# Performance work log

Hardware: AMD Instinct MI355X
Metric: run time of the kernel (lower is better)

Reference implementation:

```python
import jax, jax.numpy as jnp
import numpy as np

H = 3  # hidden size (matches nn.LSTM(3, 3, ...))


def _lstm_dir(x, Wih, Whh, bih, bhh, reverse):
    """One direction of one LSTM layer. x: [B,T,D]; PyTorch gate order i,f,g,o."""
    B = x.shape[0]
    xT = jnp.swapaxes(x, 0, 1)  # [T,B,D]
    # Precompute input projection for all timesteps (memory-bound GEMM once).
    x_proj = jnp.einsum('tbd,gd->tbg', xT, Wih) + (bih + bhh)  # [T,B,4H]

    def step(carry, xp):
        h, c = carry
        gates = xp + h @ Whh.T  # [B,4H]
        i = jax.nn.sigmoid(gates[:, :H])
        f = jax.nn.sigmoid(gates[:, H:2 * H])
        g = jnp.tanh(gates[:, 2 * H:3 * H])
        o = jax.nn.sigmoid(gates[:, 3 * H:])
        c = f * c + i * g
        h = o * jnp.tanh(c)
        return (h, c), h

    init = (jnp.zeros((B, H), x.dtype), jnp.zeros((B, H), x.dtype))
    _, hs = jax.lax.scan(step, init, x_proj, reverse=reverse)
    return jnp.swapaxes(hs, 0, 1)  # [B,T,H], time-aligned with input


def setup_inputs() -> dict:
    key = jax.random.key(0)
    ks = jax.random.split(key, 20)
    B, T = 8192, 512
    k = 1.0 / np.sqrt(H)

    def u(kk, shape):
        return jax.random.uniform(kk, shape, jnp.float32, -k, k)

    inp = {"x": jax.random.normal(ks[0], (B, T, 3), jnp.float32)}
    # layer 0: input dim 3; layer 1: input dim 2*H = 6
    inp.update({
        "W_ih_l0": u(ks[1], (4 * H, 3)),  "W_hh_l0": u(ks[2], (4 * H, H)),
        "b_ih_l0": u(ks[3], (4 * H,)),    "b_hh_l0": u(ks[4], (4 * H,)),
        "W_ih_l0r": u(ks[5], (4 * H, 3)), "W_hh_l0r": u(ks[6], (4 * H, H)),
        "b_ih_l0r": u(ks[7], (4 * H,)),   "b_hh_l0r": u(ks[8], (4 * H,)),
        "W_ih_l1": u(ks[9], (4 * H, 2 * H)),  "W_hh_l1": u(ks[10], (4 * H, H)),
        "b_ih_l1": u(ks[11], (4 * H,)),       "b_hh_l1": u(ks[12], (4 * H,)),
        "W_ih_l1r": u(ks[13], (4 * H, 2 * H)),"W_hh_l1r": u(ks[14], (4 * H, H)),
        "b_ih_l1r": u(ks[15], (4 * H,)),      "b_hh_l1r": u(ks[16], (4 * H,)),
        "W_lin": u(ks[17], (1, 2 * H)),       "b_lin": u(ks[18], (1,)),
    })
    return inp


def reference(x, W_ih_l0, W_hh_l0, b_ih_l0, b_hh_l0,
              W_ih_l0r, W_hh_l0r, b_ih_l0r, b_hh_l0r,
              W_ih_l1, W_hh_l1, b_ih_l1, b_hh_l1,
              W_ih_l1r, W_hh_l1r, b_ih_l1r, b_hh_l1r,
              W_lin, b_lin):
    # layer 0 (bidirectional)
    y0 = jnp.concatenate([
        _lstm_dir(x, W_ih_l0, W_hh_l0, b_ih_l0, b_hh_l0, False),
        _lstm_dir(x, W_ih_l0r, W_hh_l0r, b_ih_l0r, b_hh_l0r, True),
    ], axis=-1)  # [B,T,6]
    # layer 1 (bidirectional)
    y1 = jnp.concatenate([
        _lstm_dir(y0, W_ih_l1, W_hh_l1, b_ih_l1, b_hh_l1, False),
        _lstm_dir(y0, W_ih_l1r, W_hh_l1r, b_ih_l1r, b_hh_l1r, True),
    ], axis=-1)  # [B,T,6]
    last = y1[:, -1, :]  # [B,6]  (output sequence at final timestep)
    out = last @ W_lin.T + b_lin  # [B,1]
    return jax.nn.sigmoid(out.reshape(-1))  # [B]
```

## Files before the change

### kernel.cpp

```cpp
#include <hip/hip_runtime.h>


#define B_ 8192
#define T_ 512
#define LOG2E 1.4426950408889634f

typedef float v2f __attribute__((ext_vector_type(2)));

__device__ __forceinline__ float rcp_(float x)  { return __builtin_amdgcn_rcpf(x); }
__device__ __forceinline__ float exp2_(float x) { return __builtin_amdgcn_exp2f(x); }
__device__ __forceinline__ float sigm_(float x) {
  return rcp_(1.0f + exp2_(-LOG2E * x));
}
__device__ __forceinline__ float tanh_(float x) {
  return 1.0f - 2.0f * rcp_(1.0f + exp2_(2.0f * LOG2E * x));
}
__device__ __forceinline__ float act_(float p) { return rcp_(1.f + exp2_(p)); }

__device__ __forceinline__ v2f sp(float s) { return (v2f){s, s}; }
__device__ __forceinline__ v2f pkfma(v2f a, float b, v2f c) {
  return __builtin_elementwise_fma(a, sp(b), c);
}

#define PIN2(v) do {                                                      \
    double _d = __builtin_bit_cast(double, v);                            \
    asm volatile("" : "+v"(_d));                                          \
    v = __builtin_bit_cast(v2f, _d); } while (0)

template <int CTRL>
__device__ __forceinline__ float dppf(float v) {
  int s = __float_as_int(v);
  return __int_as_float(__builtin_amdgcn_update_dpp(s, s, CTRL, 0xF, 0xF, false));
}
#define QP0 dppf<0x00>
#define QP1 dppf<0x55>
#define QP2 dppf<0xAA>
#define SHL4 0x104
#define SHR4 0x114

template <bool DIRB>
__device__ __forceinline__ void l0_dir(
    const float* __restrict__ x,
    const float* __restrict__ Wi, const float* __restrict__ Wh,
    const float* __restrict__ bi, const float* __restrict__ bh,
    float* __restrict__ yout, int b, int lane)
{
  bool qgo = (lane & 4) != 0;
  int j = lane & 3; int jj = (j < 3) ? j : 0;
  const int ra = (qgo ? 6 : 0) + jj, rb = ra + 3;
  const float kx = qgo ? (-2.f * LOG2E) : (-LOG2E);
  const float ky = -LOG2E;
  const float avx = qgo ? 2.f : 1.f;
  const float dvx = qgo ? -1.f : 0.f;

  v2f w0 = {Wi[ra*3+0]*kx, Wi[rb*3+0]*ky},
      w1 = {Wi[ra*3+1]*kx, Wi[rb*3+1]*ky},
      w2 = {Wi[ra*3+2]*kx, Wi[rb*3+2]*ky};
  v2f u0 = {Wh[ra*3+0]*kx, Wh[rb*3+0]*ky},
      u1 = {Wh[ra*3+1]*kx, Wh[rb*3+1]*ky},
      u2 = {Wh[ra*3+2]*kx, Wh[rb*3+2]*ky};
  v2f b2 = {(bi[ra]+bh[ra])*kx, (bi[rb]+bh[rb])*ky};

  float h = 0.f, c = 0.f, ha0 = 0.f, ha1 = 0.f, ha2 = 0.f;
  float hs0, hs1, hs2, hs3, hs4, hs5, hs6, hs7;

  const float4* xq = (const float4*)(x + (size_t)b * (T_ * 3));
  float* ywb = yout + (size_t)b * (T_ * 3) + jj * 8;

  float4 p0, p1, p2, p3, p4, p5, q0, q1, q2, q3, q4, q5;

#define LD1(blk, R0, R1, R2, R3, R4, R5) do {                             \
    const float4* _p = xq + (blk) * 6;                                    \
    R0 = _p[0]; R1 = _p[1]; R2 = _p[2];                                   \
    R3 = _p[3]; R4 = _p[4]; R5 = _p[5];                                   \
    __builtin_amdgcn_sched_barrier(0); } while (0)

#define STEP1(x0, x1, x2, HOUT) do {                                      \
    v2f pv = pkfma(w0, (x0), b2); pv = pkfma(w1, (x1), pv);               \
    pv = pkfma(w2, (x2), pv);                                             \
    v2f uv = u0 * sp(ha0); uv = pkfma(u1, ha1, uv);                       \
    uv = pkfma(u2, ha2, uv);                                              \
    pv = pv + uv;                                                         \
    float r0v = act_(pv.x);                                               \
    float ayv = act_(pv.y);                         \
    float axv = __builtin_fmaf(avx, r0v, dvx);  \
    float slx = dppf<SHL4>(axv), sly = dppf<SHL4>(ayv);                   \
    float srx = dppf<SHR4>(axv), sry = dppf<SHR4>(ayv);                   \
    float pig = axv * (qgo ? srx : slx);           \
    float gf  = qgo ? sry : ayv;                                          \
    float gO  = qgo ? ayv : sly;                                          \
    c = __builtin_fmaf(gf, c, pig);                                       \
    float th = __builtin_fmaf(                                            \
        2.f, rcp_(1.f + exp2_(-2.f * LOG2E * c)), -1.f);                  \
    h = gO * th;                                                          \
    ha0 = QP0(h); ha1 = QP1(h); ha2 = QP2(h);                             \
    HOUT = h; } while (0)

#define S0(R0,R1,R2,R3,R4,R5) STEP1(R0.x, R0.y, R0.z, hs0)
#define S1(R0,R1,R2,R3,R4,R5) STEP1(R0.w, R1.x, R1.y, hs1)
#define S2(R0,R1,R2,R3,R4,R5) STEP1(R1.z, R1.w, R2.x, hs2)
#define S3(R0,R1,R2,R3,R4,R5) STEP1(R2.y, R2.z, R2.w, hs3)
#define S4(R0,R1,R2,R3,R4,R5) STEP1(R3.x, R3.y, R3.z, hs4)
#define S5(R0,R1,R2,R3,R4,R5) STEP1(R3.w, R4.x, R4.y, hs5)
#define S6(R0,R1,R2,R3,R4,R5) STEP1(R4.z, R4.w, R5.x, hs6)
#define S7(R0,R1,R2,R3,R4,R5) STEP1(R5.y, R5.z, R5.w, hs7)

#define PROC1(R0,R1,R2,R3,R4,R5) do {                                     \
    if (DIRB) {                                                           \
      S7(R0,R1,R2,R3,R4,R5); S6(R0,R1,R2,R3,R4,R5);                       \
      S5(R0,R1,R2,R3,R4,R5); S4(R0,R1,R2,R3,R4,R5);                       \
      S3(R0,R1,R2,R3,R4,R5); S2(R0,R1,R2,R3,R4,R5);                       \
      S1(R0,R1,R2,R3,R4,R5); S0(R0,R1,R2,R3,R4,R5);                       \
    } else {                                                              \
      S0(R0,R1,R2,R3,R4,R5); S1(R0,R1,R2,R3,R4,R5);                       \
      S2(R0,R1,R2,R3,R4,R5); S3(R0,R1,R2,R3,R4,R5);                       \
      S4(R0,R1,R2,R3,R4,R5); S5(R0,R1,R2,R3,R4,R5);                       \
      S6(R0,R1,R2,R3,R4,R5); S7(R0,R1,R2,R3,R4,R5);                       \
    } } while (0)

#define FLUSH1(blk) do {                                                  \
    if (lane < 3) {                                                       \
      float4* _o = (float4*)(ywb + (blk) * 24);                           \
      _o[0] = make_float4(hs0, hs1, hs2, hs3);                            \
      _o[1] = make_float4(hs4, hs5, hs6, hs7);                            \
    } } while (0)

#define BLK(k) (DIRB ? (63 - (k)) : (k))

  LD1(BLK(0), p0, p1, p2, p3, p4, p5);
  LD1(BLK(1), q0, q1, q2, q3, q4, q5);
  for (int k = 0; k < 64; k += 2) {
    PROC1(p0, p1, p2, p3, p4, p5);
    FLUSH1(BLK(k));
    if (k + 2 < 64) LD1(BLK(k + 2), p0, p1, p2, p3, p4, p5);
    PROC1(q0, q1, q2, q3, q4, q5);
    FLUSH1(BLK(k + 1));
    if (k + 3 < 64) LD1(BLK(k + 3), q0, q1, q2, q3, q4, q5);
  }
#undef LD1
#undef STEP1
#undef S0
#undef S1
#undef S2
#undef S3
#undef S4
#undef S5
#undef S6
#undef S7
#undef PROC1
#undef FLUSH1
#undef BLK
}

__global__ __launch_bounds__(256, 2) void lstm_l0_pair(
    const float* __restrict__ x,
    const float* __restrict__ Wf_ih, const float* __restrict__ Wf_hh,
    const float* __restrict__ bf_ih, const float* __restrict__ bf_hh,
    const float* __restrict__ Wr_ih, const float* __restrict__ Wr_hh,
    const float* __restrict__ br_ih, const float* __restrict__ br_hh,
    float* __restrict__ y0f, float* __restrict__ y0b)
{
  int gid = blockIdx.x * 256 + threadIdx.x;
  const int nfwd = B_ * 8;
  if (gid < nfwd) {
    l0_dir<false>(x, Wf_ih, Wf_hh, bf_ih, bf_hh, y0f, gid >> 3, gid & 7);
  } else {
    int g2 = gid - nfwd;
    l0_dir<true>(x, Wr_ih, Wr_hh, br_ih, br_hh, y0b, g2 >> 3, g2 & 7);
  }
}

#define CELL_TAIL(HOUT)                                                   \
    float r0v = act_(pv.x);                                               \
    float ayv = act_(pv.y);                                               \
    float axv = __builtin_fmaf(avx, r0v, dvx);                            \
    float slx = dppf<SHL4>(axv), sly = dppf<SHL4>(ayv);                   \
    float srx = dppf<SHR4>(axv), sry = dppf<SHR4>(ayv);                   \
    float pig = axv * (qgo ? srx : slx);                                  \
    float gf  = qgo ? sry : ayv;                                          \
    float gO  = qgo ? ayv : sly;                                          \
    c = __builtin_fmaf(gf, c, pig);                                       \
    float th = __builtin_fmaf(                                            \
        2.f, rcp_(1.f + exp2_(-2.f * LOG2E * c)), -1.f);                  \
    h = gO * th;                                                          \
    ha0 = QP0(h); ha1 = QP1(h); ha2 = QP2(h);                             \
    HOUT = h;

__global__ __launch_bounds__(256) void lstm_l1_fwd(
    const float* __restrict__ Wih1, const float* __restrict__ Whh1,
    const float* __restrict__ bih1, const float* __restrict__ bhh1,
    const float* __restrict__ Wih1r,
    const float* __restrict__ bih1r, const float* __restrict__ bhh1r,
    const float* __restrict__ Wlin, const float* __restrict__ blin,
    const float* __restrict__ y0f, const float* __restrict__ y0b,
    float* __restrict__ out)
{
  int tid  = blockIdx.x * 256 + threadIdx.x;
  int b    = tid >> 3;
  int lane = tid & 7;
  bool qgo = (lane & 4) != 0;
  int j = lane & 3; int jj = (j < 3) ? j : 0;
  const int ra = (qgo ? 6 : 0) + jj, rb = ra + 3;
  const float kx = qgo ? (-2.f * LOG2E) : (-LOG2E);
  const float ky = -LOG2E;
  const float avx = qgo ? 2.f : 1.f;
  const float dvx = qgo ? -1.f : 0.f;

  v2f w0 = {Wih1[ra*6+0]*kx, Wih1[rb*6+0]*ky},
      w1 = {Wih1[ra*6+1]*kx, Wih1[rb*6+1]*ky},
      w2 = {Wih1[ra*6+2]*kx, Wih1[rb*6+2]*ky},
      w3 = {Wih1[ra*6+3]*kx, Wih1[rb*6+3]*ky},
      w4 = {Wih1[ra*6+4]*kx, Wih1[rb*6+4]*ky},
      w5 = {Wih1[ra*6+5]*kx, Wih1[rb*6+5]*ky};
  v2f u0 = {Whh1[ra*3+0]*kx, Whh1[rb*3+0]*ky},
      u1 = {Whh1[ra*3+1]*kx, Whh1[rb*3+1]*ky},
      u2 = {Whh1[ra*3+2]*kx, Whh1[rb*3+2]*ky};
  v2f b2 = {(bih1[ra]+bhh1[ra])*kx, (bih1[rb]+bhh1[rb])*ky};
  PIN2(w0); PIN2(w1); PIN2(w2); PIN2(w3); PIN2(w4); PIN2(w5);
  PIN2(u0); PIN2(u1); PIN2(u2); PIN2(b2);

  const float4* yfq = (const float4*)(y0f + (size_t)b * (T_ * 3));
  const float4* ybq = (const float4*)(y0b + (size_t)b * (T_ * 3));

  const float* ufp = y0f + (size_t)b * (T_ * 3) + 63 * 24 + 7;
  const float* ubp = y0b + (size_t)b * (T_ * 3) + 63 * 24 + 7;

  float h = 0.f, c = 0.f, ha0 = 0.f, ha1 = 0.f, ha2 = 0.f;
  float hs0, hs1, hs2, hs3, hs4, hs5, hs6, hs7;
  float4 pf0, pf1, pf2, pf3, pf4, pf5, pb0, pb1, pb2, pb3, pb4, pb5;
  float4 qf0, qf1, qf2, qf3, qf4, qf5, qb0, qb1, qb2, qb3, qb4, qb5;

#define LDB(blk, F0,F1,F2,F3,F4,F5, G0,G1,G2,G3,G4,G5) do {               \
    const float4* _f = yfq + (blk) * 6;                                   \
    const float4* _g = ybq + (blk) * 6;                                   \
    F0 = _f[0]; F1 = _f[1]; F2 = _f[2];                                   \
    F3 = _f[3]; F4 = _f[4]; F5 = _f[5];                                   \
    G0 = _g[0]; G1 = _g[1]; G2 = _g[2];                                   \
    G3 = _g[3]; G4 = _g[4]; G5 = _g[5];                                   \
    __builtin_amdgcn_sched_barrier(0); } while (0)

#define STEPB(f0, f1, f2, g0, g1, g2, HOUT) do {                          \
    v2f pv = pkfma(w0, (f0), b2); pv = pkfma(w1, (f1), pv);               \
    pv = pkfma(w2, (f2), pv);                                             \
    v2f nv = w3 * sp(g0); nv = pkfma(w4, (g1), nv);                       \
    nv = pkfma(w5, (g2), nv);                                             \
    v2f uv = u0 * sp(ha0); uv = pkfma(u1, ha1, uv);                       \
    uv = pkfma(u2, ha2, uv);                                              \
    pv = (pv + nv) + uv;                                                  \
    CELL_TAIL(HOUT) } while (0)

#define PROCB(F0,F1,F2,F3,F4,F5, G0,G1,G2,G3,G4,G5) do {                  \
    STEPB(F0.x, F2.x, F4.x,  G0.x, G2.x, G4.x, hs0);                      \
    STEPB(F0.y, F2.y, F4.y,  G0.y, G2.y, G4.y, hs1);                      \
    STEPB(F0.z, F2.z, F4.z,  G0.z, G2.z, G4.z, hs2);                      \
    STEPB(F0.w, F2.w, F4.w,  G0.w, G2.w, G4.w, hs3);                      \
    STEPB(F1.x, F3.x, F5.x,  G1.x, G3.x, G5.x, hs4);                      \
    STEPB(F1.y, F3.y, F5.y,  G1.y, G3.y, G5.y, hs5);                      \
    STEPB(F1.z, F3.z, F5.z,  G1.z, G3.z, G5.z, hs6);                      \
    STEPB(F1.w, F3.w, F5.w,  G1.w, G3.w, G5.w, hs7); } while (0)

  LDB(0, pf0,pf1,pf2,pf3,pf4,pf5, pb0,pb1,pb2,pb3,pb4,pb5);
  LDB(1, qf0,qf1,qf2,qf3,qf4,qf5, qb0,qb1,qb2,qb3,qb4,qb5);
  for (int it = 0; it < 32; ++it) {
    PROCB(pf0,pf1,pf2,pf3,pf4,pf5, pb0,pb1,pb2,pb3,pb4,pb5);
    if (it < 31) LDB(2*it+2, pf0,pf1,pf2,pf3,pf4,pf5, pb0,pb1,pb2,pb3,pb4,pb5);
    PROCB(qf0,qf1,qf2,qf3,qf4,qf5, qb0,qb1,qb2,qb3,qb4,qb5);
    if (it < 31) LDB(2*it+3, qf0,qf1,qf2,qf3,qf4,qf5, qb0,qb1,qb2,qb3,qb4,qb5);
  }
  (void)hs0; (void)hs1; (void)hs2; (void)hs3;
  (void)hs4; (void)hs5; (void)hs6; (void)hs7;

  float uf0 = ufp[0], uf1 = ufp[8], uf2 = ufp[16];
  float ub0 = ubp[0], ub1 = ubp[8], ub2 = ubp[16];

  float h1b;
  {
    v2f r0 = {Wih1r[ra*6+0]*kx, Wih1r[rb*6+0]*ky},
        r1 = {Wih1r[ra*6+1]*kx, Wih1r[rb*6+1]*ky},
        r2 = {Wih1r[ra*6+2]*kx, Wih1r[rb*6+2]*ky},
        r3 = {Wih1r[ra*6+3]*kx, Wih1r[rb*6+3]*ky},
        r4 = {Wih1r[ra*6+4]*kx, Wih1r[rb*6+4]*ky},
        r5 = {Wih1r[ra*6+5]*kx, Wih1r[rb*6+5]*ky};
    v2f br = {(bih1r[ra]+bhh1r[ra])*kx, (bih1r[rb]+bhh1r[rb])*ky};
    v2f qv = pkfma(r0, uf0, br); qv = pkfma(r1, uf1, qv);
    qv = pkfma(r2, uf2, qv);     qv = pkfma(r3, ub0, qv);
    qv = pkfma(r4, ub1, qv);     qv = pkfma(r5, ub2, qv);
    float r0v = act_(qv.x);
    float ayv = act_(qv.y);
    float axv = __builtin_fmaf(avx, r0v, dvx);
    float slx = dppf<SHL4>(axv), sly = dppf<SHL4>(ayv);
    float srx = dppf<SHR4>(axv);
    float gi = qgo ? srx : axv;
    float gG = qgo ? axv : slx;
    float gO = qgo ? ayv : sly;
    float cb = gi * gG;
    h1b = gO * tanh_(cb);
  }

  float part = 0.f;
  if (!qgo && j < 3) part = __builtin_fmaf(Wlin[j], h, Wlin[3 + j] * h1b);
  part += __shfl_xor(part, 1, 8);
  part += __shfl_xor(part, 2, 8);
  part += __shfl_xor(part, 4, 8);
  if (lane == 0) out[b] = sigm_(part + blin[0]);
#undef LDB
#undef STEPB
#undef PROCB
}

extern "C" void kernel_launch(void* const* d_in, const int* in_sizes, int n_in,
                              void* d_out, int out_size, void* d_ws, size_t ws_size,
                              hipStream_t stream) {
  const float* x        = (const float*)d_in[0];
  const float* W_ih_l0  = (const float*)d_in[1];
  const float* W_hh_l0  = (const float*)d_in[2];
  const float* b_ih_l0  = (const float*)d_in[3];
  const float* b_hh_l0  = (const float*)d_in[4];
  const float* W_ih_l0r = (const float*)d_in[5];
  const float* W_hh_l0r = (const float*)d_in[6];
  const float* b_ih_l0r = (const float*)d_in[7];
  const float* b_hh_l0r = (const float*)d_in[8];
  const float* W_ih_l1  = (const float*)d_in[9];
  const float* W_hh_l1  = (const float*)d_in[10];
  const float* b_ih_l1  = (const float*)d_in[11];
  const float* b_hh_l1  = (const float*)d_in[12];
  const float* W_ih_l1r = (const float*)d_in[13];
  const float* b_ih_l1r = (const float*)d_in[15];
  const float* b_hh_l1r = (const float*)d_in[16];
  const float* W_lin    = (const float*)d_in[17];
  const float* b_lin    = (const float*)d_in[18];

  float* y0f = (float*)d_ws;
  float* y0b = (float*)d_ws + (size_t)B_ * T_ * 3;
  float* out = (float*)d_out;

  lstm_l0_pair<<<(B_ * 8 * 2) / 256, 256, 0, stream>>>(
      x, W_ih_l0, W_hh_l0, b_ih_l0, b_hh_l0,
      W_ih_l0r, W_hh_l0r, b_ih_l0r, b_hh_l0r, y0f, y0b);

  lstm_l1_fwd<<<(B_ * 8) / 256, 256, 0, stream>>>(
      W_ih_l1, W_hh_l1, b_ih_l1, b_hh_l1,
      W_ih_l1r, b_ih_l1r, b_hh_l1r,
      W_lin, b_lin, y0f, y0b, out);
}
```

Before: 166.9 us.

## Distribute per-block inputs across 8 lanes and broadcast via ds_swizzle

Before, every lane of an 8-lane sequence group loaded the full 24-float block of inputs with float4 loads, which is redundant traffic and register pressure. Now each lane loads only its slice (3 floats per timestep in layer 0, one strided element per feature in layer 1), and each timestep's values are broadcast within the group using ds_swizzle. Layer-0 weights are also pinned in registers. This cuts global/L1 load volume and VGPR use, but adds swizzle latency (LDS-path crossbar ops) into the serial recurrence chain.

```diff
diff --git a/kernel.cpp b/kernel.cpp
--- a/kernel.cpp
+++ b/kernel.cpp
@@ -37,6 +37,12 @@
 #define QP2 dppf<0xAA>
 #define SHL4 0x104
 #define SHR4 0x114
+
+template <int S>
+__device__ __forceinline__ float swz8(float v) {
+  return __int_as_float(__builtin_amdgcn_ds_swizzle(
+      __float_as_int(v), (S << 5) | 0x18));
+}
 
 template <bool DIRB>
 __device__ __forceinline__ void l0_dir(
@@ -47,6 +53,7 @@
 {
   bool qgo = (lane & 4) != 0;
   int j = lane & 3; int jj = (j < 3) ? j : 0;
+  int sl = lane & 7;
   const int ra = (qgo ? 6 : 0) + jj, rb = ra + 3;
   const float kx = qgo ? (-2.f * LOG2E) : (-LOG2E);
   const float ky = -LOG2E;
@@ -60,19 +67,19 @@
       u1 = {Wh[ra*3+1]*kx, Wh[rb*3+1]*ky},
       u2 = {Wh[ra*3+2]*kx, Wh[rb*3+2]*ky};
   v2f b2 = {(bi[ra]+bh[ra])*kx, (bi[rb]+bh[rb])*ky};
+  PIN2(w0); PIN2(w1); PIN2(w2); PIN2(u0); PIN2(u1); PIN2(u2); PIN2(b2);
 
   float h = 0.f, c = 0.f, ha0 = 0.f, ha1 = 0.f, ha2 = 0.f;
   float hs0, hs1, hs2, hs3, hs4, hs5, hs6, hs7;
 
-  const float4* xq = (const float4*)(x + (size_t)b * (T_ * 3));
+  const float* xrow = x + (size_t)b * (T_ * 3);
   float* ywb = yout + (size_t)b * (T_ * 3) + jj * 8;
 
-  float4 p0, p1, p2, p3, p4, p5, q0, q1, q2, q3, q4, q5;
-
-#define LD1(blk, R0, R1, R2, R3, R4, R5) do {                             \
-    const float4* _p = xq + (blk) * 6;                                    \
-    R0 = _p[0]; R1 = _p[1]; R2 = _p[2];                                   \
-    R3 = _p[3]; R4 = _p[4]; R5 = _p[5];                                   \
+  float ax0, ax1, ax2, bx0, bx1, bx2;
+
+#define LD1(blk, X0, X1, X2) do {                                         \
+    const float* _p = xrow + (blk) * 24 + sl * 3;                         \
+    X0 = _p[0]; X1 = _p[1]; X2 = _p[2];                                   \
     __builtin_amdgcn_sched_barrier(0); } while (0)
 
 #define STEP1(x0, x1, x2, HOUT) do {                                      \
@@ -96,30 +103,26 @@
     ha0 = QP0(h); ha1 = QP1(h); ha2 = QP2(h);                             \
     HOUT = h; } while (0)
 
-#define S0(R0,R1,R2,R3,R4,R5) STEP1(R0.x, R0.y, R0.z, hs0)
-#define S1(R0,R1,R2,R3,R4,R5) STEP1(R0.w, R1.x, R1.y, hs1)
-#define S2(R0,R1,R2,R3,R4,R5) STEP1(R1.z, R1.w, R2.x, hs2)
-#define S3(R0,R1,R2,R3,R4,R5) STEP1(R2.y, R2.z, R2.w, hs3)
-#define S4(R0,R1,R2,R3,R4,R5) STEP1(R3.x, R3.y, R3.z, hs4)
-#define S5(R0,R1,R2,R3,R4,R5) STEP1(R3.w, R4.x, R4.y, hs5)
-#define S6(R0,R1,R2,R3,R4,R5) STEP1(R4.z, R4.w, R5.x, hs6)
-#define S7(R0,R1,R2,R3,R4,R5) STEP1(R5.y, R5.z, R5.w, hs7)
-
-#define PROC1(R0,R1,R2,R3,R4,R5) do {                                     \
+#define SS0(X0,X1,X2) STEP1(swz8<0>(X0), swz8<0>(X1), swz8<0>(X2), hs0)
+#define SS1(X0,X1,X2) STEP1(swz8<1>(X0), swz8<1>(X1), swz8<1>(X2), hs1)
+#define SS2(X0,X1,X2) STEP1(swz8<2>(X0), swz8<2>(X1), swz8<2>(X2), hs2)
+#define SS3(X0,X1,X2) STEP1(swz8<3>(X0), swz8<3>(X1), swz8<3>(X2), hs3)
+#define SS4(X0,X1,X2) STEP1(swz8<4>(X0), swz8<4>(X1), swz8<4>(X2), hs4)
+#define SS5(X0,X1,X2) STEP1(swz8<5>(X0), swz8<5>(X1), swz8<5>(X2), hs5)
+#define SS6(X0,X1,X2) STEP1(swz8<6>(X0), swz8<6>(X1), swz8<6>(X2), hs6)
+#define SS7(X0,X1,X2) STEP1(swz8<7>(X0), swz8<7>(X1), swz8<7>(X2), hs7)
+
+#define PROC1(X0,X1,X2) do {                                              \
     if (DIRB) {                                                           \
-      S7(R0,R1,R2,R3,R4,R5); S6(R0,R1,R2,R3,R4,R5);                       \
-      S5(R0,R1,R2,R3,R4,R5); S4(R0,R1,R2,R3,R4,R5);                       \
-      S3(R0,R1,R2,R3,R4,R5); S2(R0,R1,R2,R3,R4,R5);                       \
-      S1(R0,R1,R2,R3,R4,R5); S0(R0,R1,R2,R3,R4,R5);                       \
+      SS7(X0,X1,X2); SS6(X0,X1,X2); SS5(X0,X1,X2); SS4(X0,X1,X2);         \
+      SS3(X0,X1,X2); SS2(X0,X1,X2); SS1(X0,X1,X2); SS0(X0,X1,X2);         \
     } else {                                                              \
-      S0(R0,R1,R2,R3,R4,R5); S1(R0,R1,R2,R3,R4,R5);                       \
-      S2(R0,R1,R2,R3,R4,R5); S3(R0,R1,R2,R3,R4,R5);                       \
-      S4(R0,R1,R2,R3,R4,R5); S5(R0,R1,R2,R3,R4,R5);                       \
-      S6(R0,R1,R2,R3,R4,R5); S7(R0,R1,R2,R3,R4,R5);                       \
+      SS0(X0,X1,X2); SS1(X0,X1,X2); SS2(X0,X1,X2); SS3(X0,X1,X2);         \
+      SS4(X0,X1,X2); SS5(X0,X1,X2); SS6(X0,X1,X2); SS7(X0,X1,X2);         \
     } } while (0)
 
 #define FLUSH1(blk) do {                                                  \
-    if (lane < 3) {                                                       \
+    if (sl < 3) {                                                         \
       float4* _o = (float4*)(ywb + (blk) * 24);                           \
       _o[0] = make_float4(hs0, hs1, hs2, hs3);                            \
       _o[1] = make_float4(hs4, hs5, hs6, hs7);                            \
@@ -127,26 +130,26 @@
 
 #define BLK(k) (DIRB ? (63 - (k)) : (k))
 
-  LD1(BLK(0), p0, p1, p2, p3, p4, p5);
-  LD1(BLK(1), q0, q1, q2, q3, q4, q5);
+  LD1(BLK(0), ax0, ax1, ax2);
+  LD1(BLK(1), bx0, bx1, bx2);
   for (int k = 0; k < 64; k += 2) {
-    PROC1(p0, p1, p2, p3, p4, p5);
+    PROC1(ax0, ax1, ax2);
     FLUSH1(BLK(k));
-    if (k + 2 < 64) LD1(BLK(k + 2), p0, p1, p2, p3, p4, p5);
-    PROC1(q0, q1, q2, q3, q4, q5);
+    if (k + 2 < 64) LD1(BLK(k + 2), ax0, ax1, ax2);
+    PROC1(bx0, bx1, bx2);
     FLUSH1(BLK(k + 1));
-    if (k + 3 < 64) LD1(BLK(k + 3), q0, q1, q2, q3, q4, q5);
+    if (k + 3 < 64) LD1(BLK(k + 3), bx0, bx1, bx2);
   }
 #undef LD1
 #undef STEP1
-#undef S0
-#undef S1
-#undef S2
-#undef S3
-#undef S4
-#undef S5
-#undef S6
-#undef S7
+#undef SS0
+#undef SS1
+#undef SS2
+#undef SS3
+#undef SS4
+#undef SS5
+#undef SS6
+#undef SS7
 #undef PROC1
 #undef FLUSH1
 #undef BLK
@@ -200,6 +203,7 @@
   int lane = tid & 7;
   bool qgo = (lane & 4) != 0;
   int j = lane & 3; int jj = (j < 3) ? j : 0;
+  int sl = lane & 7;
   const int ra = (qgo ? 6 : 0) + jj, rb = ra + 3;
   const float kx = qgo ? (-2.f * LOG2E) : (-LOG2E);
   const float ky = -LOG2E;
@@ -219,24 +223,19 @@
   PIN2(w0); PIN2(w1); PIN2(w2); PIN2(w3); PIN2(w4); PIN2(w5);
   PIN2(u0); PIN2(u1); PIN2(u2); PIN2(b2);
 
-  const float4* yfq = (const float4*)(y0f + (size_t)b * (T_ * 3));
-  const float4* ybq = (const float4*)(y0b + (size_t)b * (T_ * 3));
-
-  const float* ufp = y0f + (size_t)b * (T_ * 3) + 63 * 24 + 7;
-  const float* ubp = y0b + (size_t)b * (T_ * 3) + 63 * 24 + 7;
+  const float* yfr = y0f + (size_t)b * (T_ * 3);
+  const float* ybr = y0b + (size_t)b * (T_ * 3);
 
   float h = 0.f, c = 0.f, ha0 = 0.f, ha1 = 0.f, ha2 = 0.f;
   float hs0, hs1, hs2, hs3, hs4, hs5, hs6, hs7;
-  float4 pf0, pf1, pf2, pf3, pf4, pf5, pb0, pb1, pb2, pb3, pb4, pb5;
-  float4 qf0, qf1, qf2, qf3, qf4, qf5, qb0, qb1, qb2, qb3, qb4, qb5;
-
-#define LDB(blk, F0,F1,F2,F3,F4,F5, G0,G1,G2,G3,G4,G5) do {               \
-    const float4* _f = yfq + (blk) * 6;                                   \
-    const float4* _g = ybq + (blk) * 6;                                   \
-    F0 = _f[0]; F1 = _f[1]; F2 = _f[2];                                   \
-    F3 = _f[3]; F4 = _f[4]; F5 = _f[5];                                   \
-    G0 = _g[0]; G1 = _g[1]; G2 = _g[2];                                   \
-    G3 = _g[3]; G4 = _g[4]; G5 = _g[5];                                   \
+  float af0, af1, af2, ag0, ag1, ag2;
+  float bf0, bf1, bf2, bg0, bg1, bg2;
+
+#define LDB(blk, F0,F1,F2, G0,G1,G2) do {                                 \
+    const float* _f = yfr + (blk) * 24 + sl;                              \
+    const float* _g = ybr + (blk) * 24 + sl;                              \
+    F0 = _f[0]; F1 = _f[8]; F2 = _f[16];                                  \
+    G0 = _g[0]; G1 = _g[8]; G2 = _g[16];                                  \
     __builtin_amdgcn_sched_barrier(0); } while (0)
 
 #define STEPB(f0, f1, f2, g0, g1, g2, HOUT) do {                          \
@@ -249,27 +248,33 @@
     pv = (pv + nv) + uv;                                                  \
     CELL_TAIL(HOUT) } while (0)
 
-#define PROCB(F0,F1,F2,F3,F4,F5, G0,G1,G2,G3,G4,G5) do {                  \
-    STEPB(F0.x, F2.x, F4.x,  G0.x, G2.x, G4.x, hs0);                      \
-    STEPB(F0.y, F2.y, F4.y,  G0.y, G2.y, G4.y, hs1);                      \
-    STEPB(F0.z, F2.z, F4.z,  G0.z, G2.z, G4.z, hs2);                      \
-    STEPB(F0.w, F2.w, F4.w,  G0.w, G2.w, G4.w, hs3);                      \
-    STEPB(F1.x, F3.x, F5.x,  G1.x, G3.x, G5.x, hs4);                      \
-    STEPB(F1.y, F3.y, F5.y,  G1.y, G3.y, G5.y, hs5);                      \
-    STEPB(F1.z, F3.z, F5.z,  G1.z, G3.z, G5.z, hs6);                      \
-    STEPB(F1.w, F3.w, F5.w,  G1.w, G3.w, G5.w, hs7); } while (0)
-
-  LDB(0, pf0,pf1,pf2,pf3,pf4,pf5, pb0,pb1,pb2,pb3,pb4,pb5);
-  LDB(1, qf0,qf1,qf2,qf3,qf4,qf5, qb0,qb1,qb2,qb3,qb4,qb5);
+#define SB(s, HS, F0,F1,F2, G0,G1,G2)                                     \
+    STEPB(swz8<s>(F0), swz8<s>(F1), swz8<s>(F2),                          \
+          swz8<s>(G0), swz8<s>(G1), swz8<s>(G2), HS)
+
+#define PROCB(F0,F1,F2, G0,G1,G2) do {                                    \
+    SB(0, hs0, F0,F1,F2, G0,G1,G2);                                       \
+    SB(1, hs1, F0,F1,F2, G0,G1,G2);                                       \
+    SB(2, hs2, F0,F1,F2, G0,G1,G2);                                       \
+    SB(3, hs3, F0,F1,F2, G0,G1,G2);                                       \
+    SB(4, hs4, F0,F1,F2, G0,G1,G2);                                       \
+    SB(5, hs5, F0,F1,F2, G0,G1,G2);                                       \
+    SB(6, hs6, F0,F1,F2, G0,G1,G2);                                       \
+    SB(7, hs7, F0,F1,F2, G0,G1,G2); } while (0)
+
+  LDB(0, af0,af1,af2, ag0,ag1,ag2);
+  LDB(1, bf0,bf1,bf2, bg0,bg1,bg2);
   for (int it = 0; it < 32; ++it) {
-    PROCB(pf0,pf1,pf2,pf3,pf4,pf5, pb0,pb1,pb2,pb3,pb4,pb5);
-    if (it < 31) LDB(2*it+2, pf0,pf1,pf2,pf3,pf4,pf5, pb0,pb1,pb2,pb3,pb4,pb5);
-    PROCB(qf0,qf1,qf2,qf3,qf4,qf5, qb0,qb1,qb2,qb3,qb4,qb5);
-    if (it < 31) LDB(2*it+3, qf0,qf1,qf2,qf3,qf4,qf5, qb0,qb1,qb2,qb3,qb4,qb5);
+    PROCB(af0,af1,af2, ag0,ag1,ag2);
+    if (it < 31) LDB(2*it+2, af0,af1,af2, ag0,ag1,ag2);
+    PROCB(bf0,bf1,bf2, bg0,bg1,bg2);
+    if (it < 31) LDB(2*it+3, bf0,bf1,bf2, bg0,bg1,bg2);
   }
   (void)hs0; (void)hs1; (void)hs2; (void)hs3;
   (void)hs4; (void)hs5; (void)hs6; (void)hs7;
 
+  const float* ufp = yfr + 63 * 24 + 7;
+  const float* ubp = ybr + 63 * 24 + 7;
   float uf0 = ufp[0], uf1 = ufp[8], uf2 = ufp[16];
   float ub0 = ubp[0], ub1 = ubp[8], ub2 = ubp[16];
 
@@ -305,6 +310,7 @@
   if (lane == 0) out[b] = sigm_(part + blin[0]);
 #undef LDB
 #undef STEPB
+#undef SB
 #undef PROCB
 }
 
```

Measured after the change: 189.9 us. 13.8% more time.
